# Kernel optimization log

Hardware: AMD Instinct MI355X
Metric: run time of the kernel (lower is better)

## Reference

```python
import jax, jax.numpy as jnp
import numpy as np
import math

NUM_USER, NUM_COURSE, NUM_TEACHER, NUM_SCHOOL = 100000, 10000, 5000, 3000
D = 16
B, LS, LT, LSC = 1024, 200, 10, 5
NC, LU, LS2, LT2 = 100, 50, 3, 5


def setup_inputs() -> dict:
    key = jax.random.key(0)
    ks = jax.random.split(key, 32)
    sig = 1.0 / D  # torch init: normal(0, 1/num_dim) on ALL params (overwrites padding row too)
    p = lambda k, shp: jax.random.normal(k, shp, jnp.float32) * sig
    ri = lambda k, shp, hi: jax.random.randint(k, shp, 0, hi)
    inp = {}
    inp['user_idx']       = ri(ks[0], (B, 1), NUM_USER)
    inp['user_sequence']  = ri(ks[1], (B, LS), NUM_COURSE + 1)   # may hit padding idx
    inp['user_teachers']  = ri(ks[2], (B, LT), NUM_TEACHER + 1)
    inp['user_school']    = ri(ks[3], (B, LSC), NUM_SCHOOL + 1)
    inp['user_len_seq']     = jax.random.randint(ks[4], (B, 1), 1, LS + 1).astype(jnp.float32)
    inp['user_len_teacher'] = jax.random.randint(ks[5], (B, 1), 1, LT + 1).astype(jnp.float32)
    inp['user_len_school']  = jax.random.randint(ks[6], (B, 1), 1, LSC + 1).astype(jnp.float32)
    inp['course_set']     = ri(ks[7], (B, NC), NUM_COURSE)
    inp['course_user']    = ri(ks[8], (B, NC, LU), NUM_USER + 1)
    inp['course_school']  = ri(ks[9], (B, NC, LS2), NUM_SCHOOL + 1)
    inp['course_teacher'] = ri(ks[10], (B, NC, LT2), NUM_TEACHER + 1)
    inp['course_len_u']       = jax.random.randint(ks[11], (B, NC), 1, LU + 1).astype(jnp.float32)
    inp['course_len_teacher'] = jax.random.randint(ks[12], (B, NC), 1, LT2 + 1).astype(jnp.float32)
    # learned parameters (jax layout: Linear weight is [in, out])
    inp['user_table']    = p(ks[13], (NUM_USER + 1, D))
    inp['course_table']  = p(ks[14], (NUM_COURSE + 1, D))
    inp['teacher_table'] = p(ks[15], (NUM_TEACHER + 1, D))
    inp['school_table']  = p(ks[16], (NUM_SCHOOL + 1, D))
    inp['Qw'] = p(ks[17], (D, D)); inp['Qb'] = p(ks[18], (D,))
    inp['Kw'] = p(ks[19], (D, D)); inp['Kb'] = p(ks[20], (D,))
    inp['g1w'] = p(ks[21], (2 * D, D)); inp['g1b'] = p(ks[22], (D,))
    inp['g2w'] = p(ks[23], (D, D));     inp['g2b'] = p(ks[24], (D,))
    inp['caw1'] = p(ks[25], (D, D)); inp['cab1'] = p(ks[26], (D,))
    inp['caw2'] = p(ks[27], (D, 1))
    return inp


def _transformer(x, Qw, Qb, Kw, Kb):
    # x: [B, L, d] -> [B, d]. Faithful to source: K is RESHAPED (not transposed) to [B, d, L].
    b, L, d = x.shape
    Q = jax.nn.relu(x @ Qw + Qb)                       # [B, L, d]
    K = jax.nn.relu(x @ Kw + Kb).reshape(b, d, L)      # reshape, as in source
    s = jnp.matmul(Q, K) / math.sqrt(d)                # [B, L, L]
    s = jnp.where(jnp.eye(L, dtype=bool), jnp.float32(1e-32), s)  # diag set to 1e-32
    su = jax.nn.softmax(s, axis=2)
    a = jnp.matmul(su, x)                              # [B, L, d]
    return a.mean(axis=1)


def reference(user_idx, user_sequence, user_teachers, user_school,
              user_len_seq, user_len_teacher, user_len_school,
              course_set, course_user, course_school, course_teacher,
              course_len_u, course_len_teacher,
              user_table, course_table, teacher_table, school_table,
              Qw, Qb, Kw, Kb, g1w, g1b, g2w, g2b, caw1, cab1, caw2):
    # ---- user side ----
    user_emb = user_table[user_idx[:, 0]]                       # [B, d]
    seq_emb = course_table[user_sequence]                       # [B, LS, d]
    seq_rep = _transformer(seq_emb, Qw, Qb, Kw, Kb)             # [B, d]
    ut_mean = teacher_table[user_teachers].sum(axis=1) / user_len_teacher
    us_mean = school_table[user_school].sum(axis=1) / user_len_school
    agg = (seq_rep + ut_mean + us_mean) / 3.0
    h = jnp.concatenate([user_emb, agg], axis=1)                # [B, 2d]
    user_final = jax.nn.relu(h @ g1w + g1b) @ g2w + g2b         # [B, d]
    # ---- course side ----
    course_emb = course_table[course_set]                       # [B, Nc, d]
    cu_mean = user_table[course_user].sum(axis=2) / course_len_u[..., None]
    cs_sum  = school_table[course_school].sum(axis=2)           # note: no division (as in source)
    ct_mean = teacher_table[course_teacher].sum(axis=2) / course_len_teacher[..., None]
    nb = jnp.stack([cu_mean, cs_sum, ct_mean], axis=2)          # [B, Nc, 3, d]
    att = jax.nn.softmax(jax.nn.sigmoid(nb @ caw1 + cab1) @ caw2, axis=2)
    _course_agg = (nb * att).sum(axis=2)  # computed in source but unused (dead code)
    # ---- score ----
    out = jnp.sum(user_final[:, None, :] * course_emb, axis=2)  # [B, Nc]
    return out
```

## Files before the change

kernel.cpp:

```cpp
#include <hip/hip_runtime.h>
#include <hip/hip_bf16.h>

#define NBATCH 1024
#define LSEQ   200
#define DD     16
#define LTT    10
#define LSCH   5
#define NCC    100

#define XT_S   232
#define QB_S   24
#define KT_S   24
#define WT_S   20

#define QSCALE 0.3606737602f

typedef __bf16 bf16_4 __attribute__((ext_vector_type(4)));
typedef float  f32x4  __attribute__((ext_vector_type(4)));
typedef short  short4v __attribute__((ext_vector_type(4)));
typedef unsigned int uint2v __attribute__((ext_vector_type(2)));

__device__ __forceinline__ int kswz(int j) { return ((j >> 3) ^ (j >> 6)) & 1; }

__device__ __forceinline__ f32x4 mfma16(bf16_4 a, bf16_4 b, f32x4 c) {
#if __has_builtin(__builtin_amdgcn_mfma_f32_16x16x16bf16_1k)
    return __builtin_amdgcn_mfma_f32_16x16x16bf16_1k(
        __builtin_bit_cast(short4v, a), __builtin_bit_cast(short4v, b), c, 0, 0, 0);
#else
    uint2v au = __builtin_bit_cast(uint2v, a);
    uint2v bu = __builtin_bit_cast(uint2v, b);
    asm("v_mfma_f32_16x16x16_bf16 %0, %1, %2, %0" : "+v"(c) : "v"(au), "v"(bu));
    return c;
#endif
}

__global__ __launch_bounds__(256, 4) void hin_kernel(
    const int*   __restrict__ user_idx,
    const int*   __restrict__ user_sequence,
    const int*   __restrict__ user_teachers,
    const int*   __restrict__ user_school,
    const float* __restrict__ user_len_teacher,
    const float* __restrict__ user_len_school,
    const int*   __restrict__ course_set,
    const float* __restrict__ user_table,
    const float* __restrict__ course_table,
    const float* __restrict__ teacher_table,
    const float* __restrict__ school_table,
    const float* __restrict__ Qw, const float* __restrict__ Qb,
    const float* __restrict__ Kw, const float* __restrict__ Kb,
    const float* __restrict__ g1w, const float* __restrict__ g1b,
    const float* __restrict__ g2w, const float* __restrict__ g2b,
    float*       __restrict__ out)
{
    __shared__ __align__(16) __bf16 xt[DD * XT_S];
    __shared__ __align__(16) __bf16 qb[208 * QB_S];
    __shared__ __align__(16) __bf16 kt[208 * KT_S];
    __shared__ __align__(16) __bf16 wqt[DD * WT_S], wkt[DD * WT_S];
    __shared__ float bQv[DD], bKv[DD];
    __shared__ float red[4][DD];
    __shared__ __align__(16) float tot12t[64];
    __shared__ float uf[DD];
    __shared__ float gst[800];
    __shared__ float rows_pre[256];
    __shared__ float lens[2];

    const int b    = blockIdx.x;
    const int t    = threadIdx.x;
    const int w    = t >> 6;
    const int lane = t & 63;
    const int grp  = lane >> 4;
    const int li   = lane & 15;

    {
        const int k = t >> 4, n = t & 15;
        wqt[n*WT_S + k] = (__bf16)Qw[k*DD + n];
        wkt[n*WT_S + k] = (__bf16)Kw[k*DD + n];
    }
    if (t < DD) { bQv[t] = Qb[t]; bKv[t] = Kb[t]; }
    if (t < 128)
        xt[(t >> 3)*XT_S + 200 + (t & 7)] = (__bf16)0.f;
    else {
        const int i = t - 128;
        kt[(200 + (i >> 4))*KT_S + (i & 15)] = (__bf16)0.f;
    }
    for (int i = t; i < 800; i += 256) {
        float v;
        if      (i < 512) v = g1w[i];
        else if (i < 528) v = g1b[i - 512];
        else if (i < 784) v = g2w[i - 528];
        else              v = g2b[i - 784];
        gst[i] = v;
    }
    if (t < 16)       rows_pre[t] = user_table[user_idx[b]*DD + t];
    else if (t < 176) { const int i = t - 16;
        rows_pre[t] = teacher_table[user_teachers[b*LTT + (i >> 4)]*DD + (i & 15)]; }
    else if (t < 256) { const int i = t - 176;
        rows_pre[t] = school_table[user_school[b*LSCH + (i >> 4)]*DD + (i & 15)]; }
    if (t == 0) { lens[0] = user_len_teacher[b]; lens[1] = user_len_school[b]; }

    for (int e = t; e < 800; e += 256) {
        const int l = e >> 2, dq = e & 3;
        const int idx = user_sequence[b*LSEQ + l];
        const float4 v = *(const float4*)&course_table[idx*DD + dq*4];
        xt[(dq*4+0)*XT_S + l] = (__bf16)v.x;
        xt[(dq*4+1)*XT_S + l] = (__bf16)v.y;
        xt[(dq*4+2)*XT_S + l] = (__bf16)v.z;
        xt[(dq*4+3)*XT_S + l] = (__bf16)v.w;
    }
    __syncthreads();

    {
        float qbias[4];
        #pragma unroll
        for (int r = 0; r < 4; r++) qbias[r] = bQv[grp*4 + r];
        const float kbias = bKv[li];
        const bf16_4 wq = *(const bf16_4*)&wqt[li*WT_S + grp*4];
        const bf16_4 wk = *(const bf16_4*)&wkt[li*WT_S + grp*4];
        for (int mt = w; mt < 13; mt += 4) {
            const int l0 = mt * 16;
            bf16_4 xf;
            #pragma unroll
            for (int e = 0; e < 4; e++)
                xf[e] = xt[(grp*4 + e)*XT_S + l0 + li];
            const f32x4 zc = {0.f, 0.f, 0.f, 0.f};
            f32x4 qv = mfma16(wq, xf, zc);
            f32x4 kv = mfma16(xf, wk, zc);
            bf16_4 qpk;
            #pragma unroll
            for (int r = 0; r < 4; r++)
                qpk[r] = (__bf16)(QSCALE * fmaxf(qv[r] + qbias[r], 0.f));
            *(bf16_4*)&qb[(l0 + li)*QB_S + grp*4] = qpk;
            #pragma unroll
            for (int r = 0; r < 4; r++) {
                const int lrow = l0 + grp*4 + r;
                if (lrow < LSEQ) {
                    const float val = fmaxf(kv[r] + kbias, 0.f);
                    const int f = lrow*DD + li;
                    const int p = f / 200;
                    const int j = f - p*200;
                    kt[j*KT_S + (p ^ (kswz(j) << 3))] = (__bf16)val;
                }
            }
        }
    }
    __syncthreads();

    const int wu = __builtin_amdgcn_readfirstlane(w);
    const int dr = li - grp*4;

    bf16_4 onesb;
    #pragma unroll
    for (int i = 0; i < 4; i++) onesb[i] = (__bf16)1.0f;

    bf16_4 kfr[13], xbr[13];
    #pragma unroll
    for (int jt = 0; jt < 13; jt++) {
        const int jr = jt*16 + li;
        kfr[jt] = *(const bf16_4*)&kt[jr*KT_S + ((grp*4) ^ (kswz(jr) << 3))];
        xbr[jt] = *(const bf16_4*)&xt[li*XT_S + jt*16 + grp*4];
    }

    float wsum = 0.f;

    #pragma unroll
    for (int mi = 0; mi < 3; mi++) {
        const int mt = wu + mi*4;
        const int m0 = mt * 16;
        const bf16_4 qf = *(const bf16_4*)&qb[(m0 + li)*QB_S + grp*4];

        f32x4 acc0 = {0.f, 0.f, 0.f, 0.f};
        f32x4 acc1 = {0.f, 0.f, 0.f, 0.f};
        f32x4 accD = {0.f, 0.f, 0.f, 0.f};

        #pragma unroll
        for (int jt = 0; jt < 13; jt++) {
            const f32x4 zc = {0.f, 0.f, 0.f, 0.f};
            f32x4 s = mfma16(kfr[jt], qf, zc);
            bf16_4 pa;
            #pragma unroll
            for (int r = 0; r < 4; r++) {
                float pv = __builtin_amdgcn_exp2f(s[r]);
                if (jt == 12 && grp >= 2) pv = 0.f;
                if (jt == mt && dr == r)  pv = 1.0f;
                pa[r] = (__bf16)pv;
            }
            accD = mfma16(pa, onesb, accD);
            if (jt & 1) acc1 = mfma16(pa, xbr[jt], acc1);
            else        acc0 = mfma16(pa, xbr[jt], acc0);
        }

        #pragma unroll
        for (int r = 0; r < 4; r++)
            wsum += (acc0[r] + acc1[r]) * __builtin_amdgcn_rcpf(accD[r]);
    }

    f32x4 acc12 = {0.f, 0.f, 0.f, 0.f};
    {
        const int jlo = (wu == 0) ? 0 : (3*wu + 1);
        const int jhi = 3*wu + 4;
        const bf16_4 qf = *(const bf16_4*)&qb[(192 + li)*QB_S + grp*4];
        f32x4 accD = {0.f, 0.f, 0.f, 0.f};
        #pragma unroll
        for (int jt = 0; jt < 13; jt++) {
            if (jt >= jlo && jt < jhi) {
                const f32x4 zc = {0.f, 0.f, 0.f, 0.f};
                f32x4 s = mfma16(kfr[jt], qf, zc);
                bf16_4 pa;
                #pragma unroll
                for (int r = 0; r < 4; r++) {
                    float pv = __builtin_amdgcn_exp2f(s[r]);
                    if (jt == 12 && grp >= 2) pv = 0.f;
                    if (jt == 12 && dr == r)  pv = 1.0f;
                    pa[r] = (__bf16)pv;
                }
                accD  = mfma16(pa, onesb, accD);
                acc12 = mfma16(pa, xbr[jt], acc12);
            }
        }
        if (li == 0) {
            #pragma unroll
            for (int r = 0; r < 4; r++)
                tot12t[(grp*4 + r)*4 + w] = accD[r];
        }
    }
    __syncthreads();

    #pragma unroll
    for (int r = 0; r < 4; r++) {
        const int q = grp*4 + r;
        const float4 p4 = *(const float4*)&tot12t[q*4];
        const float dsum = (p4.x + p4.y) + (p4.z + p4.w);
        const float a = acc12[r] * __builtin_amdgcn_rcpf(dsum);
        wsum += (192 + q < LSEQ) ? a : 0.f;
    }

    wsum += __shfl_xor(wsum, 16);
    wsum += __shfl_xor(wsum, 32);
    if (lane < DD) red[w][lane] = wsum;
    __syncthreads();

    float4 ce0, ce1, ce2, ce3;
    if (t < NCC) {
        const int ci = course_set[b*NCC + t];
        const float* ce = &course_table[ci*DD];
        ce0 = *(const float4*)&ce[0];
        ce1 = *(const float4*)&ce[4];
        ce2 = *(const float4*)&ce[8];
        ce3 = *(const float4*)&ce[12];
    }

    if (w == 0) {
        const float ue  = rows_pre[li];
        const float seq = (red[0][li] + red[1][li] + red[2][li] + red[3][li]) * (1.0f / LSEQ);
        float uts = 0.f;
        #pragma unroll
        for (int i = 0; i < LTT; i++)  uts += rows_pre[16 + i*16 + li];
        float uss = 0.f;
        #pragma unroll
        for (int i = 0; i < LSCH; i++) uss += rows_pre[176 + i*16 + li];
        const float agg = (seq + uts / lens[0] + uss / lens[1]) * (1.0f / 3.0f);
        float a1 = gst[512 + li];
        #pragma unroll
        for (int k = 0; k < 16; k++) a1 = fmaf(__shfl(ue,  k), gst[k*DD + li], a1);
        #pragma unroll
        for (int k = 0; k < 16; k++) a1 = fmaf(__shfl(agg, k), gst[(16 + k)*DD + li], a1);
        const float hidv = fmaxf(a1, 0.f);
        float a2 = gst[784 + li];
        #pragma unroll
        for (int k = 0; k < 16; k++) a2 = fmaf(__shfl(hidv, k), gst[528 + k*DD + li], a2);
        if (lane < DD) uf[lane] = a2;
    }
    __syncthreads();

    if (t < NCC) {
        const float4 u0 = *(const float4*)&uf[0];
        const float4 u1 = *(const float4*)&uf[4];
        const float4 u2 = *(const float4*)&uf[8];
        const float4 u3 = *(const float4*)&uf[12];
        float s = ce0.x*u0.x + ce0.y*u0.y + ce0.z*u0.z + ce0.w*u0.w;
        s      += ce1.x*u1.x + ce1.y*u1.y + ce1.z*u1.z + ce1.w*u1.w;
        s      += ce2.x*u2.x + ce2.y*u2.y + ce2.z*u2.z + ce2.w*u2.w;
        s      += ce3.x*u3.x + ce3.y*u3.y + ce3.z*u3.z + ce3.w*u3.w;
        out[b*NCC + t] = s;
    }
}

extern "C" void kernel_launch(void* const* d_in, const int* in_sizes, int n_in,
                              void* d_out, int out_size, void* d_ws, size_t ws_size,
                              hipStream_t stream) {
    const int*   user_idx         = (const int*)  d_in[0];
    const int*   user_sequence    = (const int*)  d_in[1];
    const int*   user_teachers    = (const int*)  d_in[2];
    const int*   user_school      = (const int*)  d_in[3];
    const float* user_len_teacher = (const float*)d_in[5];
    const float* user_len_school  = (const float*)d_in[6];
    const int*   course_set       = (const int*)  d_in[7];
    const float* user_table       = (const float*)d_in[13];
    const float* course_table     = (const float*)d_in[14];
    const float* teacher_table    = (const float*)d_in[15];
    const float* school_table     = (const float*)d_in[16];
    const float* Qw  = (const float*)d_in[17];
    const float* Qb  = (const float*)d_in[18];
    const float* Kw  = (const float*)d_in[19];
    const float* Kb  = (const float*)d_in[20];
    const float* g1w = (const float*)d_in[21];
    const float* g1b = (const float*)d_in[22];
    const float* g2w = (const float*)d_in[23];
    const float* g2b = (const float*)d_in[24];

    float* outp = (float*)d_out;

    hipLaunchKernelGGL(hin_kernel, dim3(NBATCH), dim3(256), 0, stream,
                       user_idx, user_sequence, user_teachers, user_school,
                       user_len_teacher, user_len_school, course_set,
                       user_table, course_table, teacher_table, school_table,
                       Qw, Qb, Kw, Kb, g1w, g1b, g2w, g2b, outp);
}
```

Before: 20.93 us.

## Keep Q fragments in registers and interleave all query tiles in one loop

Drops the shared-memory Q buffer: each wave computes its own Q tiles (including the tail tile 192) directly into registers, and only the K scatter goes to shared memory. The three query-tile attention loops and the tail loop are merged into one jt loop, so independent MFMA and exp chains from four tiles interleave for more instruction-level parallelism. The cost is more live registers (four sets of accumulators) and a redundant Q computation for the tail tile on every wave.

```diff
diff --git a/kernel.cpp b/kernel.cpp
--- a/kernel.cpp
+++ b/kernel.cpp
@@ -9,7 +9,6 @@
 #define NCC    100
 
 #define XT_S   232
-#define QB_S   24
 #define KT_S   24
 #define WT_S   20
 
@@ -53,7 +52,6 @@
     float*       __restrict__ out)
 {
     __shared__ __align__(16) __bf16 xt[DD * XT_S];
-    __shared__ __align__(16) __bf16 qb[208 * QB_S];
     __shared__ __align__(16) __bf16 kt[208 * KT_S];
     __shared__ __align__(16) __bf16 wqt[DD * WT_S], wkt[DD * WT_S];
     __shared__ float bQv[DD], bKv[DD];
@@ -109,6 +107,10 @@
     }
     __syncthreads();
 
+    const int wu = __builtin_amdgcn_readfirstlane(w);
+    const int dr = li - grp*4;
+
+    bf16_4 qf0, qf1, qf2, qf12;
     {
         float qbias[4];
         #pragma unroll
@@ -116,8 +118,8 @@
         const float kbias = bKv[li];
         const bf16_4 wq = *(const bf16_4*)&wqt[li*WT_S + grp*4];
         const bf16_4 wk = *(const bf16_4*)&wkt[li*WT_S + grp*4];
-        for (int mt = w; mt < 13; mt += 4) {
-            const int l0 = mt * 16;
+
+        auto compute_qk = [&](int l0, bf16_4& qout, bool do_scatter) {
             bf16_4 xf;
             #pragma unroll
             for (int e = 0; e < 4; e++)
@@ -125,28 +127,29 @@
             const f32x4 zc = {0.f, 0.f, 0.f, 0.f};
             f32x4 qv = mfma16(wq, xf, zc);
             f32x4 kv = mfma16(xf, wk, zc);
-            bf16_4 qpk;
             #pragma unroll
             for (int r = 0; r < 4; r++)
-                qpk[r] = (__bf16)(QSCALE * fmaxf(qv[r] + qbias[r], 0.f));
-            *(bf16_4*)&qb[(l0 + li)*QB_S + grp*4] = qpk;
-            #pragma unroll
-            for (int r = 0; r < 4; r++) {
-                const int lrow = l0 + grp*4 + r;
-                if (lrow < LSEQ) {
-                    const float val = fmaxf(kv[r] + kbias, 0.f);
-                    const int f = lrow*DD + li;
-                    const int p = f / 200;
-                    const int j = f - p*200;
-                    kt[j*KT_S + (p ^ (kswz(j) << 3))] = (__bf16)val;
+                qout[r] = (__bf16)(QSCALE * fmaxf(qv[r] + qbias[r], 0.f));
+            if (do_scatter) {
+                #pragma unroll
+                for (int r = 0; r < 4; r++) {
+                    const int lrow = l0 + grp*4 + r;
+                    if (lrow < LSEQ) {
+                        const float val = fmaxf(kv[r] + kbias, 0.f);
+                        const int f = lrow*DD + li;
+                        const int p = f / 200;
+                        const int j = f - p*200;
+                        kt[j*KT_S + (p ^ (kswz(j) << 3))] = (__bf16)val;
+                    }
                 }
             }
-        }
-    }
-    __syncthreads();
-
-    const int wu = __builtin_amdgcn_readfirstlane(w);
-    const int dr = li - grp*4;
+        };
+        compute_qk(wu*16,       qf0, true);
+        compute_qk((wu+4)*16,   qf1, true);
+        compute_qk((wu+8)*16,   qf2, true);
+        compute_qk(192,         qf12, wu == 0);
+    }
+    __syncthreads();
 
     bf16_4 onesb;
     #pragma unroll
@@ -160,68 +163,61 @@
         xbr[jt] = *(const bf16_4*)&xt[li*XT_S + jt*16 + grp*4];
     }
 
-    float wsum = 0.f;
-
-    #pragma unroll
-    for (int mi = 0; mi < 3; mi++) {
-        const int mt = wu + mi*4;
-        const int m0 = mt * 16;
-        const bf16_4 qf = *(const bf16_4*)&qb[(m0 + li)*QB_S + grp*4];
-
-        f32x4 acc0 = {0.f, 0.f, 0.f, 0.f};
-        f32x4 acc1 = {0.f, 0.f, 0.f, 0.f};
-        f32x4 accD = {0.f, 0.f, 0.f, 0.f};
-
-        #pragma unroll
-        for (int jt = 0; jt < 13; jt++) {
-            const f32x4 zc = {0.f, 0.f, 0.f, 0.f};
-            f32x4 s = mfma16(kfr[jt], qf, zc);
-            bf16_4 pa;
+    const int mt0 = wu, mt1 = wu + 4, mt2 = wu + 8;
+    const int jlo = (wu == 0) ? 0 : (3*wu + 1);
+    const int jhi = 3*wu + 4;
+
+    f32x4 ao0 = {0.f,0.f,0.f,0.f}, aD0 = {0.f,0.f,0.f,0.f};
+    f32x4 ao1 = {0.f,0.f,0.f,0.f}, aD1 = {0.f,0.f,0.f,0.f};
+    f32x4 ao2 = {0.f,0.f,0.f,0.f}, aD2 = {0.f,0.f,0.f,0.f};
+    f32x4 ao3 = {0.f,0.f,0.f,0.f}, aD3 = {0.f,0.f,0.f,0.f};
+
+    #pragma unroll
+    for (int jt = 0; jt < 13; jt++) {
+        const f32x4 zc = {0.f, 0.f, 0.f, 0.f};
+        f32x4 s0 = mfma16(kfr[jt], qf0, zc);
+        f32x4 s1 = mfma16(kfr[jt], qf1, zc);
+        f32x4 s2 = mfma16(kfr[jt], qf2, zc);
+        bf16_4 p0, p1, p2;
+        #pragma unroll
+        for (int r = 0; r < 4; r++) {
+            float v0 = __builtin_amdgcn_exp2f(s0[r]);
+            float v1 = __builtin_amdgcn_exp2f(s1[r]);
+            float v2 = __builtin_amdgcn_exp2f(s2[r]);
+            if (jt == 12 && grp >= 2) { v0 = 0.f; v1 = 0.f; v2 = 0.f; }
+            if (jt == mt0 && dr == r) v0 = 1.0f;
+            if (jt == mt1 && dr == r) v1 = 1.0f;
+            if (jt == mt2 && dr == r) v2 = 1.0f;
+            p0[r] = (__bf16)v0; p1[r] = (__bf16)v1; p2[r] = (__bf16)v2;
+        }
+        aD0 = mfma16(p0, onesb, aD0);  ao0 = mfma16(p0, xbr[jt], ao0);
+        aD1 = mfma16(p1, onesb, aD1);  ao1 = mfma16(p1, xbr[jt], ao1);
+        aD2 = mfma16(p2, onesb, aD2);  ao2 = mfma16(p2, xbr[jt], ao2);
+        if (jt >= jlo && jt < jhi) {
+            f32x4 s3 = mfma16(kfr[jt], qf12, zc);
+            bf16_4 p3;
             #pragma unroll
             for (int r = 0; r < 4; r++) {
-                float pv = __builtin_amdgcn_exp2f(s[r]);
-                if (jt == 12 && grp >= 2) pv = 0.f;
-                if (jt == mt && dr == r)  pv = 1.0f;
-                pa[r] = (__bf16)pv;
+                float v3 = __builtin_amdgcn_exp2f(s3[r]);
+                if (jt == 12 && grp >= 2) v3 = 0.f;
+                if (jt == 12 && dr == r)  v3 = 1.0f;
+                p3[r] = (__bf16)v3;
             }
-            accD = mfma16(pa, onesb, accD);
-            if (jt & 1) acc1 = mfma16(pa, xbr[jt], acc1);
-            else        acc0 = mfma16(pa, xbr[jt], acc0);
+            aD3 = mfma16(p3, onesb, aD3);  ao3 = mfma16(p3, xbr[jt], ao3);
         }
-
+    }
+
+    float wsum = 0.f;
+    #pragma unroll
+    for (int r = 0; r < 4; r++) {
+        wsum += ao0[r] * __builtin_amdgcn_rcpf(aD0[r]);
+        wsum += ao1[r] * __builtin_amdgcn_rcpf(aD1[r]);
+        wsum += ao2[r] * __builtin_amdgcn_rcpf(aD2[r]);
+    }
+    if (li == 0) {
         #pragma unroll
         for (int r = 0; r < 4; r++)
-            wsum += (acc0[r] + acc1[r]) * __builtin_amdgcn_rcpf(accD[r]);
-    }
-
-    f32x4 acc12 = {0.f, 0.f, 0.f, 0.f};
-    {
-        const int jlo = (wu == 0) ? 0 : (3*wu + 1);
-        const int jhi = 3*wu + 4;
-        const bf16_4 qf = *(const bf16_4*)&qb[(192 + li)*QB_S + grp*4];
-        f32x4 accD = {0.f, 0.f, 0.f, 0.f};
-        #pragma unroll
-        for (int jt = 0; jt < 13; jt++) {
-            if (jt >= jlo && jt < jhi) {
-                const f32x4 zc = {0.f, 0.f, 0.f, 0.f};
-                f32x4 s = mfma16(kfr[jt], qf, zc);
-                bf16_4 pa;
-                #pragma unroll
-                for (int r = 0; r < 4; r++) {
-                    float pv = __builtin_amdgcn_exp2f(s[r]);
-                    if (jt == 12 && grp >= 2) pv = 0.f;
-                    if (jt == 12 && dr == r)  pv = 1.0f;
-                    pa[r] = (__bf16)pv;
-                }
-                accD  = mfma16(pa, onesb, accD);
-                acc12 = mfma16(pa, xbr[jt], acc12);
-            }
-        }
-        if (li == 0) {
-            #pragma unroll
-            for (int r = 0; r < 4; r++)
-                tot12t[(grp*4 + r)*4 + w] = accD[r];
-        }
+            tot12t[(grp*4 + r)*4 + w] = aD3[r];
     }
     __syncthreads();
 
@@ -230,8 +226,8 @@
         const int q = grp*4 + r;
         const float4 p4 = *(const float4*)&tot12t[q*4];
         const float dsum = (p4.x + p4.y) + (p4.z + p4.w);
-        const float a = acc12[r] * __builtin_amdgcn_rcpf(dsum);
-        wsum += (192 + q < LSEQ) ? a : 0.f;
+        if (192 + q < LSEQ)
+            wsum += ao3[r] * __builtin_amdgcn_rcpf(dsum);
     }
 
     wsum += __shfl_xor(wsum, 16);
```

After: 20.73 us. About the same (-1.0%).
